# Optimization experiments

Hardware: AMD Instinct MI355X
Metric: run time of the kernel (lower is better)

Reference implementation:

```python
import jax, jax.numpy as jnp
import numpy as np
from jax import lax

CIN, COUT, K, PAD = 256, 128, 3, 1


def setup_inputs() -> dict:
    key = jax.random.key(0)
    ks = jax.random.split(key, 5)
    N, h0, w0 = 2, 64, 64
    x = jax.random.normal(ks[0], (N, CIN, h0, w0), jnp.float32)
    lateral_feat = jax.random.normal(ks[1], (N, COUT, 1, 1), jnp.float32)
    trans_w = jax.random.normal(ks[2], (CIN, COUT, K, K), jnp.float32) * 0.02
    off_w1 = jax.random.normal(ks[3], (64, COUT, 3, 3), jnp.float32) * 0.02
    off_b1 = jnp.zeros((64,), jnp.float32)
    off_w2 = jax.random.normal(ks[4], (2 * K * K, 64, 3, 3), jnp.float32) * 0.02
    off_b2 = jnp.zeros((2 * K * K,), jnp.float32)
    return dict(x=x, lateral_feat=lateral_feat, trans_w=trans_w,
                off_w1=off_w1, off_b1=off_b1, off_w2=off_w2, off_b2=off_b2)


def _conv2d(x, w, b, pad):
    y = lax.conv_general_dilated(x, w, (1, 1), [(pad, pad), (pad, pad)],
                                 dimension_numbers=('NCHW', 'OIHW', 'NCHW'))
    return y + b[None, :, None, None]


def _conv_transpose2d(x, w, stride, pad, out_pad):
    # torch ConvTranspose2d weight layout: [Cin, Cout, k, k]
    k = w.shape[2]
    wt = jnp.flip(w, (2, 3)).transpose(1, 0, 2, 3)  # [Cout, Cin, k, k]
    lo = k - 1 - pad
    hi = k - 1 - pad + out_pad
    return lax.conv_general_dilated(x, wt, (1, 1), [(lo, hi), (lo, hi)],
                                    lhs_dilation=(stride, stride),
                                    dimension_numbers=('NCHW', 'OIHW', 'NCHW'))


def _deform_conv2d(x, offset, w, pad):
    # x [N,C,H,W], offset [N,2*K*K,H,W] (y,x interleaved per kernel tap), w [O,C,K,K]
    N, C, H, W = x.shape
    O = w.shape[0]
    KK = K * K
    off = offset.reshape(N, KK, 2, H, W)
    ky = jnp.arange(KK) // K
    kx = jnp.arange(KK) % K
    py = jnp.arange(H)[None, None, :, None] + (ky - pad)[None, :, None, None] + off[:, :, 0]
    px = jnp.arange(W)[None, None, None, :] + (kx - pad)[None, :, None, None] + off[:, :, 1]
    y0 = jnp.floor(py)
    x0 = jnp.floor(px)
    dy = py - y0
    dx = px - x0
    y0i = y0.astype(jnp.int32)
    x0i = x0.astype(jnp.int32)
    xf = x.reshape(N, C, H * W)

    def corner(yi, xi, wgt):
        valid = (yi >= 0) & (yi < H) & (xi >= 0) & (xi < W)
        idx = (jnp.clip(yi, 0, H - 1) * W + jnp.clip(xi, 0, W - 1)).reshape(N, -1)
        v = jnp.take_along_axis(xf, idx[:, None, :], axis=2).reshape(N, C, KK, H, W)
        return v * (wgt * valid)[:, None]

    sampled = (corner(y0i, x0i, (1 - dy) * (1 - dx))
               + corner(y0i, x0i + 1, (1 - dy) * dx)
               + corner(y0i + 1, x0i, dy * (1 - dx))
               + corner(y0i + 1, x0i + 1, dy * dx))  # [N,C,KK,H,W]
    return jnp.einsum('nckhw,ock->nohw', sampled, w.reshape(O, C, KK))


def reference(x, lateral_feat, trans_w, off_w1, off_b1, off_w2, off_b2):
    up = _conv_transpose2d(x, trans_w, 2, PAD, 1)          # [N, COUT, 2h0, 2w0]
    h = jax.nn.relu(_conv2d(lateral_feat, off_w1, off_b1, 1))
    offset = jnp.tanh(_conv2d(h, off_w2, off_b2, 1))       # [N, 18, 1, 1]
    N, C, H, W = up.shape
    # offset.repeat(1, 1, H, W) with 1x1 spatial input == broadcast to full grid
    offset = jnp.broadcast_to(offset, (N, 2 * K * K, H, W))
    # deform_conv2d uses trans_conv weight [O=CIN, I=COUT, K, K], stride=1, pad=PAD
    return _deform_conv2d(up, offset, trans_w, PAD)        # [N, CIN, H, W]
```

## Files before the change

### kernel.cpp

```cpp
#include <hip/hip_runtime.h>
#include <hip/hip_bf16.h>
#include <math.h>

typedef __attribute__((ext_vector_type(8))) short s16x8;
typedef __attribute__((ext_vector_type(4))) float f32x4;

__device__ __forceinline__ unsigned short f2bf(float f) {
    union { float f; unsigned int u; } v; v.f = f;
    unsigned int u = v.u + 0x7FFFu + ((v.u >> 16) & 1u);
    return (unsigned short)(u >> 16);
}
__device__ __forceinline__ unsigned pk2(float lo, float hi) {
    __hip_bfloat162 h = __float22bfloat162_rn(make_float2(lo, hi));
    union { __hip_bfloat162 h; unsigned u; } v; v.h = h;
    return v.u;
}
__device__ __forceinline__ float blo(unsigned u) {
    union { unsigned u; float f; } v; v.u = u << 16; return v.f;
}
__device__ __forceinline__ float bhi(unsigned u) {
    union { unsigned u; float f; } v; v.u = u & 0xffff0000u; return v.f;
}

__device__ __forceinline__ void blend_store(uint4 uA, uint4 uB, uint4 uC, uint4 uD,
                                            float4 cw, unsigned short* dst) {
    unsigned ua[4] = {uA.x, uA.y, uA.z, uA.w};
    unsigned ub[4] = {uB.x, uB.y, uB.z, uB.w};
    unsigned uc[4] = {uC.x, uC.y, uC.z, uC.w};
    unsigned ud[4] = {uD.x, uD.y, uD.z, uD.w};
    unsigned pk[4];
#pragma unroll
    for (int i = 0; i < 4; ++i) {
        float vL = cw.x * blo(ua[i]) + cw.y * blo(ub[i]) + cw.z * blo(uc[i]) + cw.w * blo(ud[i]);
        float vH = cw.x * bhi(ua[i]) + cw.y * bhi(ub[i]) + cw.z * bhi(uc[i]) + cw.w * bhi(ud[i]);
        pk[i] = pk2(vL, vH);
    }
    *(uint4*)dst = make_uint4(pk[0], pk[1], pk[2], pk[3]);
}

__global__ __launch_bounds__(256) void k_prep(const float* __restrict__ x,
                                              const float* __restrict__ lat,
                                              const float* __restrict__ tw,
                                              const float* __restrict__ w1,
                                              const float* __restrict__ b1,
                                              const float* __restrict__ w2,
                                              const float* __restrict__ b2,
                                              unsigned short* __restrict__ xp,
                                              unsigned short* __restrict__ A2f,
                                              unsigned short* __restrict__ Awf,
                                              int* __restrict__ ipar,
                                              float* __restrict__ fpar) {
    __shared__ float sm[8420];
    int b = blockIdx.x, t = threadIdx.x;
    if (b == 0) {
        for (int i = t; i < 8192; i += 256) sm[(i >> 7) * 129 + (i & 127)] = w1[i * 9 + 4];
        __syncthreads();
        if (t < 128) {
            int n = t >> 6, o = t & 63;
            float s = b1[o];
            const float* ln = lat + n * 128;
#pragma unroll 8
            for (int c = 0; c < 128; ++c) s += ln[c] * sm[o * 129 + c];
            sm[8256 + t] = fmaxf(s, 0.f);
        }
        __syncthreads();
        if (t < 36) {
            int n = t / 18, j = t % 18;
            float s = b2[j];
            for (int o = 0; o < 64; ++o) s += sm[8256 + n * 64 + o] * w2[(j * 64 + o) * 9 + 4];
            float ov = tanhf(s);
            ov = fminf(fmaxf(ov, -0.999999f), 0.999999f);
            sm[8384 + t] = ov;
        }
        __syncthreads();
        if (t < 36) {
            int n = t / 18, j = t % 18;
            int tap = j >> 1, d = j & 1;
            float ov = sm[8384 + t];
            float fl = floorf(ov);
            int kc = d ? (tap % 3) : (tap / 3);
            ipar[(n * 9 + tap) * 2 + d] = kc - 1 + (int)fl;
            fpar[(n * 9 + tap) * 2 + d] = ov - fl;
        }
    } else if (b < 145) {
        int slot = (b - 1) * 256 + t;
        int l = slot & 63;
        int mi = (slot >> 6) & 3;
        int w = (slot >> 8) & 3;
        int k = slot >> 10;
        int row = w * 64 + mi * 16 + (l & 15);
        int kq = l >> 4;
        unsigned short v[8];
#pragma unroll
        for (int j = 0; j < 8; ++j) {
            int kcol = k * 32 + kq * 8 + j;
            int tap = kcol >> 7, c = kcol & 127;
            v[j] = f2bf(tw[(row * 128 + c) * 9 + tap]);
        }
        unsigned p0 = (unsigned)v[0] | ((unsigned)v[1] << 16);
        unsigned p1 = (unsigned)v[2] | ((unsigned)v[3] << 16);
        unsigned p2 = (unsigned)v[4] | ((unsigned)v[5] << 16);
        unsigned p3 = (unsigned)v[6] | ((unsigned)v[7] << 16);
        *(uint4*)(A2f + slot * 8) = make_uint4(p0, p1, p2, p3);
    } else if (b < 289) {
        int slot = (b - 145) * 256 + t;
        int l = slot & 63;
        int mi = (slot >> 6) & 3;
        int wm = (slot >> 8) & 1;
        int k = slot >> 9;
        int row = wm * 64 + mi * 16 + (l & 15);
        int kq = l >> 4;
        unsigned short v[8];
#pragma unroll
        for (int j = 0; j < 8; ++j) {
            int kcol = k * 32 + kq * 8 + j;
            int t9 = kcol >> 8, ci = kcol & 255;
            int ky = t9 / 3, kx = t9 - ky * 3;
            v[j] = f2bf(tw[(ci * 128 + row) * 9 + (2 - ky) * 3 + (2 - kx)]);
        }
        unsigned p0 = (unsigned)v[0] | ((unsigned)v[1] << 16);
        unsigned p1 = (unsigned)v[2] | ((unsigned)v[3] << 16);
        unsigned p2 = (unsigned)v[4] | ((unsigned)v[5] << 16);
        unsigned p3 = (unsigned)v[6] | ((unsigned)v[7] << 16);
        *(uint4*)(Awf + slot * 8) = make_uint4(p0, p1, p2, p3);
    } else {
        int bb = b - 289;
        int h = bb & 63, cq = (bb >> 6) & 3, n = bb >> 8;
        int c0 = cq * 64;
        {
            int wcol = t & 63, sub = t >> 6;
            for (int r = 0; r < 16; ++r) {
                int ci_l = r * 4 + sub;
                sm[ci_l * 65 + wcol] = x[((n * 256 + c0 + ci_l) * 64 + h) * 64 + wcol];
            }
        }
        __syncthreads();
        int wcol = t >> 2, cg = t & 3;
        unsigned short* dst = xp + (size_t)n * (65 * 65 * 256) + (h * 65 + wcol) * 256 + c0 + cg * 16;
        unsigned pk[8];
#pragma unroll
        for (int j = 0; j < 8; ++j)
            pk[j] = pk2(sm[(cg * 16 + 2 * j) * 65 + wcol], sm[(cg * 16 + 2 * j + 1) * 65 + wcol]);
        *(uint4*)dst = make_uint4(pk[0], pk[1], pk[2], pk[3]);
        *(uint4*)(dst + 8) = make_uint4(pk[4], pk[5], pk[6], pk[7]);
    }
}

__global__ __launch_bounds__(256) void k_tconv3(const unsigned short* __restrict__ xp,
                                                const unsigned short* __restrict__ Awf,
                                                unsigned short* __restrict__ upp) {
    __shared__ unsigned short Bs[2][64][40];
    __shared__ int st9[4];
    __shared__ int sbb[4];
    int t = threadIdx.x;
    int b = blockIdx.x;
    int phase = b >> 8, jj = b & 255;
    int n = jj >> 7, xpar = ((jj >> 6) & 1) ^ phase, yh = jj & 63;
    int y = yh * 2 + phase;
    const unsigned short* xpn = xp + (size_t)n * (65 * 65 * 256);

    int lane = t & 63, w = t >> 6;
    int col = lane & 15, q = lane >> 4;
    int wm = w >> 1, wn = w & 1;
    int bx = t >> 2, bcg = t & 3;
    int boff = bx * 256 + bcg * 8;

    int kys[2], kxs[2], nky, nkx;
    if (phase) { kys[0] = 0; kys[1] = 2; nky = 2; } else { kys[0] = 1; kys[1] = 1; nky = 1; }
    if (xpar)  { kxs[0] = 0; kxs[1] = 2; nkx = 2; } else { kxs[0] = 1; kxs[1] = 1; nkx = 1; }
    int nslots = nky * nkx;
    if (t < nslots) {
        int a1 = t / nkx, a2 = t % nkx;
        int ky = kys[a1], kx = kxs[a2];
        st9[t] = ky * 3 + kx;
        int d2 = (y + ky - 1) >> 1;
        int s = (xpar + kx - 1) >> 1;
        sbb[t] = (d2 * 65 + s) * 256;
    }
    int NT = nslots * 8;

    f32x4 acc[4][2];
#pragma unroll
    for (int mi = 0; mi < 4; ++mi)
#pragma unroll
        for (int ni = 0; ni < 2; ++ni) acc[mi][ni] = (f32x4){0.f, 0.f, 0.f, 0.f};

    __syncthreads();

    const unsigned short* Afw = Awf + wm * 2048 + lane * 8;
    s16x8 a_cur[4], a_nxt[4];

    {
        int kAw0 = st9[0] * 8;
        uint4 bv = *(const uint4*)(xpn + sbb[0] + boff);
        *(uint4*)&Bs[0][bx][bcg * 8] = bv;
#pragma unroll
        for (int mi = 0; mi < 4; ++mi)
            a_cur[mi] = *(const s16x8*)(Afw + kAw0 * 4096 + mi * 512);
    }
    __syncthreads();

    for (int cc = 0; cc < NT; ++cc) {
        int cc1 = cc + 1;
        uint4 bv;
        if (cc1 < NT) {
            int slot1 = cc1 >> 3, cb1 = cc1 & 7;
            int t9v = st9[slot1];
            int base = sbb[slot1];
            bv = *(const uint4*)(xpn + base + cb1 * 32 + boff);
            int kAw1 = t9v * 8 + cb1;
#pragma unroll
            for (int mi = 0; mi < 4; ++mi)
                a_nxt[mi] = *(const s16x8*)(Afw + kAw1 * 4096 + mi * 512);
        }
        s16x8 bb[2];
#pragma unroll
        for (int ni = 0; ni < 2; ++ni)
            bb[ni] = *(const s16x8*)&Bs[cc & 1][wn * 32 + ni * 16 + col][q * 8];
#pragma unroll
        for (int mi = 0; mi < 4; ++mi)
#pragma unroll
            for (int ni = 0; ni < 2; ++ni)
                acc[mi][ni] = __builtin_amdgcn_mfma_f32_16x16x32_bf16(a_cur[mi], bb[ni], acc[mi][ni], 0, 0, 0);
        if (cc1 < NT) {
            *(uint4*)&Bs[cc1 & 1][bx][bcg * 8] = bv;
#pragma unroll
            for (int mi = 0; mi < 4; ++mi) a_cur[mi] = a_nxt[mi];
        }
        __syncthreads();
    }

    unsigned short* uppn = upp + (size_t)n * (132 * 132 * 128);
#pragma unroll
    for (int mi = 0; mi < 4; ++mi)
#pragma unroll
        for (int ni = 0; ni < 2; ++ni) {
            int co = wm * 64 + mi * 16 + q * 4;
            int p64 = wn * 32 + ni * 16 + col;
            int xg = 2 * p64 + xpar;
            unsigned short* p = uppn + ((y + 2) * 132 + (xg + 2)) * 128 + co;
            unsigned lo = pk2(acc[mi][ni][0], acc[mi][ni][1]);
            unsigned hi = pk2(acc[mi][ni][2], acc[mi][ni][3]);
            *(uint2*)p = make_uint2(lo, hi);
        }
}

__global__ __launch_bounds__(256) void k_deform3(const unsigned short* __restrict__ upp,
                                                 const unsigned short* __restrict__ A2f,
                                                 const int* __restrict__ ipar,
                                                 const float* __restrict__ fpar,
                                                 float* __restrict__ out) {
    __shared__ unsigned short Bs[2][64][40];
    __shared__ int sbase[9];
    __shared__ float4 swt[9];
    int t = threadIdx.x;
    int b = blockIdx.x;
    int xcd = b & 7, j = b >> 3;
    int n = xcd >> 2, band = xcd & 3;
    int y = band * 32 + (j & 31);
    int tx0 = (j >> 5) * 64;
    const unsigned short* uppn = upp + (size_t)n * (132 * 132 * 128);

    int lane = t & 63, w = t >> 6;
    int col = lane & 15, q = lane >> 4;
    int bx = t >> 2, bcg = t & 3;
    int boff = bx * 128 + bcg * 8;

    if (t < 9) {
        int iy = ipar[(n * 9 + t) * 2 + 0], ix = ipar[(n * 9 + t) * 2 + 1];
        float fy = fpar[(n * 9 + t) * 2 + 0], fx = fpar[(n * 9 + t) * 2 + 1];
        sbase[t] = ((y + 2 + iy) * 132 + (tx0 + 2 + ix)) * 128;
        swt[t] = make_float4((1.f - fy) * (1.f - fx), (1.f - fy) * fx, fy * (1.f - fx), fy * fx);
    }

    f32x4 acc[4][4];
#pragma unroll
    for (int mi = 0; mi < 4; ++mi)
#pragma unroll
        for (int ni = 0; ni < 4; ++ni) acc[mi][ni] = (f32x4){0.f, 0.f, 0.f, 0.f};

    __syncthreads();

    const unsigned short* Afw = A2f + w * 2048 + lane * 8;
    s16x8 a_cur[4], a_nxt[4];

    {
        const unsigned short* p = uppn + sbase[0] + boff;
        uint4 uA = *(const uint4*)p;
        uint4 uB = *(const uint4*)(p + 128);
        uint4 uC = *(const uint4*)(p + 16896);
        uint4 uD = *(const uint4*)(p + 17024);
        blend_store(uA, uB, uC, uD, swt[0], &Bs[0][bx][bcg * 8]);
#pragma unroll
        for (int mi = 0; mi < 4; ++mi)
            a_cur[mi] = *(const s16x8*)(Afw + mi * 512);
    }
    __syncthreads();

#pragma unroll 2
    for (int k = 0; k < 36; ++k) {
        int k1 = k + 1;
        uint4 uA, uB, uC, uD;
        float4 cw;
        if (k1 < 36) {
            int t1 = k1 >> 2, cb1 = (k1 & 3) * 32;
            int base = sbase[t1];
            cw = swt[t1];
            const unsigned short* p = uppn + base + cb1 + boff;
            uA = *(const uint4*)p;
            uB = *(const uint4*)(p + 128);
            uC = *(const uint4*)(p + 16896);
            uD = *(const uint4*)(p + 17024);
#pragma unroll
            for (int mi = 0; mi < 4; ++mi)
                a_nxt[mi] = *(const s16x8*)(Afw + k1 * 8192 + mi * 512);
        }
        s16x8 bb[4];
#pragma unroll
        for (int ni = 0; ni < 4; ++ni)
            bb[ni] = *(const s16x8*)&Bs[k & 1][ni * 16 + col][q * 8];
#pragma unroll
        for (int mi = 0; mi < 4; ++mi)
#pragma unroll
            for (int ni = 0; ni < 4; ++ni)
                acc[mi][ni] = __builtin_amdgcn_mfma_f32_16x16x32_bf16(a_cur[mi], bb[ni], acc[mi][ni], 0, 0, 0);
        if (k1 < 36) {
            blend_store(uA, uB, uC, uD, cw, &Bs[k1 & 1][bx][bcg * 8]);
#pragma unroll
            for (int mi = 0; mi < 4; ++mi) a_cur[mi] = a_nxt[mi];
        }
        __syncthreads();
    }

#pragma unroll
    for (int mi = 0; mi < 4; ++mi)
#pragma unroll
        for (int ni = 0; ni < 4; ++ni) {
            int o = w * 64 + mi * 16 + q * 4;
            int xg = tx0 + ni * 16 + col;
            float* p = out + (((size_t)(n * 256 + o)) * 128 + y) * 128 + xg;
            p[0]         = acc[mi][ni][0];
            p[16384]     = acc[mi][ni][1];
            p[2 * 16384] = acc[mi][ni][2];
            p[3 * 16384] = acc[mi][ni][3];
        }
}

extern "C" void kernel_launch(void* const* d_in, const int* in_sizes, int n_in,
                              void* d_out, int out_size, void* d_ws, size_t ws_size,
                              hipStream_t stream) {
    const float* x   = (const float*)d_in[0];
    const float* lat = (const float*)d_in[1];
    const float* tw  = (const float*)d_in[2];
    const float* w1  = (const float*)d_in[3];
    const float* b1  = (const float*)d_in[4];
    const float* w2  = (const float*)d_in[5];
    const float* b2  = (const float*)d_in[6];
    float* out = (float*)d_out;

    char* ws = (char*)d_ws;
    unsigned short* upp = (unsigned short*)ws;
    unsigned short* xp  = (unsigned short*)(ws + 8921088);
    unsigned short* A2f = (unsigned short*)(ws + 13247488);
    unsigned short* Awf = (unsigned short*)(ws + 13837312);
    int*   ipar         = (int*)(ws + 14427136);
    float* fpar         = (float*)(ws + 14427424);

    hipMemsetAsync(ws, 0, 13247488, stream);
    k_prep<<<801, 256, 0, stream>>>(x, lat, tw, w1, b1, w2, b2, xp, A2f, Awf, ipar, fpar);
    k_tconv3<<<512, 256, 0, stream>>>(xp, Awf, upp);
    k_deform3<<<512, 256, 0, stream>>>(upp, A2f, ipar, fpar, out);
}
```

Before: 150.4 us.

## Restructure tconv to register-direct MFMA and deepen deform pipeline

```diff
diff --git a/kernel.cpp b/kernel.cpp
--- a/kernel.cpp
+++ b/kernel.cpp
@@ -4,6 +4,7 @@
 
 typedef __attribute__((ext_vector_type(8))) short s16x8;
 typedef __attribute__((ext_vector_type(4))) float f32x4;
+typedef __attribute__((ext_vector_type(2))) float v2f;
 
 __device__ __forceinline__ unsigned short f2bf(float f) {
     union { float f; unsigned int u; } v; v.f = f;
@@ -15,15 +16,15 @@
     union { __hip_bfloat162 h; unsigned u; } v; v.h = h;
     return v.u;
 }
-__device__ __forceinline__ float blo(unsigned u) {
-    union { unsigned u; float f; } v; v.u = u << 16; return v.f;
-}
-__device__ __forceinline__ float bhi(unsigned u) {
-    union { unsigned u; float f; } v; v.u = u & 0xffff0000u; return v.f;
-}
-
-__device__ __forceinline__ void blend_store(uint4 uA, uint4 uB, uint4 uC, uint4 uD,
-                                            float4 cw, unsigned short* dst) {
+__device__ __forceinline__ v2f up2(unsigned u) {
+    union { unsigned u; float f; } a, b;
+    a.u = u << 16; b.u = u & 0xffff0000u;
+    v2f r; r.x = a.f; r.y = b.f; return r;
+}
+
+__device__ __forceinline__ void blend4(uint4 uA, uint4 uB, uint4 uC, uint4 uD,
+                                       v2f c00, v2f c01, v2f c10, v2f c11,
+                                       unsigned short* dst) {
     unsigned ua[4] = {uA.x, uA.y, uA.z, uA.w};
     unsigned ub[4] = {uB.x, uB.y, uB.z, uB.w};
     unsigned uc[4] = {uC.x, uC.y, uC.z, uC.w};
@@ -31,9 +32,8 @@
     unsigned pk[4];
 #pragma unroll
     for (int i = 0; i < 4; ++i) {
-        float vL = cw.x * blo(ua[i]) + cw.y * blo(ub[i]) + cw.z * blo(uc[i]) + cw.w * blo(ud[i]);
-        float vH = cw.x * bhi(ua[i]) + cw.y * bhi(ub[i]) + cw.z * bhi(uc[i]) + cw.w * bhi(ud[i]);
-        pk[i] = pk2(vL, vH);
+        v2f r = c00 * up2(ua[i]) + c01 * up2(ub[i]) + c10 * up2(uc[i]) + c11 * up2(ud[i]);
+        pk[i] = pk2(r.x, r.y);
     }
     *(uint4*)dst = make_uint4(pk[0], pk[1], pk[2], pk[3]);
 }
@@ -146,113 +146,73 @@
     }
 }
 
-__global__ __launch_bounds__(256) void k_tconv3(const unsigned short* __restrict__ xp,
+__global__ __launch_bounds__(256) void k_tconv4(const unsigned short* __restrict__ xp,
                                                 const unsigned short* __restrict__ Awf,
                                                 unsigned short* __restrict__ upp) {
-    __shared__ unsigned short Bs[2][64][40];
-    __shared__ int st9[4];
-    __shared__ int sbb[4];
     int t = threadIdx.x;
     int b = blockIdx.x;
-    int phase = b >> 8, jj = b & 255;
-    int n = jj >> 7, xpar = ((jj >> 6) & 1) ^ phase, yh = jj & 63;
-    int y = yh * 2 + phase;
+    int cls = b >> 7;
+    int phase = (cls < 2) ? 1 : 0;
+    int xpar = 1 - (cls & 1);
+    int idx = b & 127;
+    int n = idx >> 6, yh = idx & 63;
+    int y = 2 * yh + phase;
     const unsigned short* xpn = xp + (size_t)n * (65 * 65 * 256);
 
     int lane = t & 63, w = t >> 6;
     int col = lane & 15, q = lane >> 4;
-    int wm = w >> 1, wn = w & 1;
-    int bx = t >> 2, bcg = t & 3;
-    int boff = bx * 256 + bcg * 8;
-
-    int kys[2], kxs[2], nky, nkx;
-    if (phase) { kys[0] = 0; kys[1] = 2; nky = 2; } else { kys[0] = 1; kys[1] = 1; nky = 1; }
-    if (xpar)  { kxs[0] = 0; kxs[1] = 2; nkx = 2; } else { kxs[0] = 1; kxs[1] = 1; nkx = 1; }
-    int nslots = nky * nkx;
-    if (t < nslots) {
-        int a1 = t / nkx, a2 = t % nkx;
-        int ky = kys[a1], kx = kxs[a2];
-        st9[t] = ky * 3 + kx;
+    int pos = w * 16 + col;
+
+    int nky = phase ? 2 : 1;
+    int nkx = xpar ? 2 : 1;
+
+    f32x4 acc[8];
+#pragma unroll
+    for (int mi = 0; mi < 8; ++mi) acc[mi] = (f32x4){0.f, 0.f, 0.f, 0.f};
+
+    const unsigned short* Afl = Awf + lane * 8;
+
+    for (int a1 = 0; a1 < nky; ++a1) {
+        int ky = phase ? (a1 ? 2 : 0) : 1;
         int d2 = (y + ky - 1) >> 1;
-        int s = (xpar + kx - 1) >> 1;
-        sbb[t] = (d2 * 65 + s) * 256;
-    }
-    int NT = nslots * 8;
-
-    f32x4 acc[4][2];
-#pragma unroll
-    for (int mi = 0; mi < 4; ++mi)
-#pragma unroll
-        for (int ni = 0; ni < 2; ++ni) acc[mi][ni] = (f32x4){0.f, 0.f, 0.f, 0.f};
-
-    __syncthreads();
-
-    const unsigned short* Afw = Awf + wm * 2048 + lane * 8;
-    s16x8 a_cur[4], a_nxt[4];
-
-    {
-        int kAw0 = st9[0] * 8;
-        uint4 bv = *(const uint4*)(xpn + sbb[0] + boff);
-        *(uint4*)&Bs[0][bx][bcg * 8] = bv;
-#pragma unroll
-        for (int mi = 0; mi < 4; ++mi)
-            a_cur[mi] = *(const s16x8*)(Afw + kAw0 * 4096 + mi * 512);
-    }
-    __syncthreads();
-
-    for (int cc = 0; cc < NT; ++cc) {
-        int cc1 = cc + 1;
-        uint4 bv;
-        if (cc1 < NT) {
-            int slot1 = cc1 >> 3, cb1 = cc1 & 7;
-            int t9v = st9[slot1];
-            int base = sbb[slot1];
-            bv = *(const uint4*)(xpn + base + cb1 * 32 + boff);
-            int kAw1 = t9v * 8 + cb1;
-#pragma unroll
-            for (int mi = 0; mi < 4; ++mi)
-                a_nxt[mi] = *(const s16x8*)(Afw + kAw1 * 4096 + mi * 512);
-        }
-        s16x8 bb[2];
-#pragma unroll
-        for (int ni = 0; ni < 2; ++ni)
-            bb[ni] = *(const s16x8*)&Bs[cc & 1][wn * 32 + ni * 16 + col][q * 8];
-#pragma unroll
-        for (int mi = 0; mi < 4; ++mi)
-#pragma unroll
-            for (int ni = 0; ni < 2; ++ni)
-                acc[mi][ni] = __builtin_amdgcn_mfma_f32_16x16x32_bf16(a_cur[mi], bb[ni], acc[mi][ni], 0, 0, 0);
-        if (cc1 < NT) {
-            *(uint4*)&Bs[cc1 & 1][bx][bcg * 8] = bv;
-#pragma unroll
-            for (int mi = 0; mi < 4; ++mi) a_cur[mi] = a_nxt[mi];
-        }
-        __syncthreads();
+        for (int a2 = 0; a2 < nkx; ++a2) {
+            int kx = xpar ? (a2 ? 2 : 0) : 1;
+            int s = (xpar + kx - 1) >> 1;
+            int t9 = ky * 3 + kx;
+            const unsigned short* bptr = xpn + ((size_t)(d2 * 65 + s + pos)) * 256 + q * 8;
+            const unsigned short* aptr = Afl + t9 * 8 * 4096;
+#pragma unroll 2
+            for (int cb = 0; cb < 8; ++cb) {
+                s16x8 bf = *(const s16x8*)(bptr + cb * 32);
+                s16x8 a[8];
+#pragma unroll
+                for (int mi = 0; mi < 8; ++mi)
+                    a[mi] = *(const s16x8*)(aptr + cb * 4096 + (mi >> 2) * 2048 + (mi & 3) * 512);
+#pragma unroll
+                for (int mi = 0; mi < 8; ++mi)
+                    acc[mi] = __builtin_amdgcn_mfma_f32_16x16x32_bf16(a[mi], bf, acc[mi], 0, 0, 0);
+            }
+        }
     }
 
     unsigned short* uppn = upp + (size_t)n * (132 * 132 * 128);
-#pragma unroll
-    for (int mi = 0; mi < 4; ++mi)
-#pragma unroll
-        for (int ni = 0; ni < 2; ++ni) {
-            int co = wm * 64 + mi * 16 + q * 4;
-            int p64 = wn * 32 + ni * 16 + col;
-            int xg = 2 * p64 + xpar;
-            unsigned short* p = uppn + ((y + 2) * 132 + (xg + 2)) * 128 + co;
-            unsigned lo = pk2(acc[mi][ni][0], acc[mi][ni][1]);
-            unsigned hi = pk2(acc[mi][ni][2], acc[mi][ni][3]);
-            *(uint2*)p = make_uint2(lo, hi);
-        }
-}
-
-__global__ __launch_bounds__(256) void k_deform3(const unsigned short* __restrict__ upp,
-                                                 const unsigned short* __restrict__ A2f,
-                                                 const int* __restrict__ ipar,
-                                                 const float* __restrict__ fpar,
-                                                 float* __restrict__ out) {
-    __shared__ unsigned short Bs[2][64][40];
-    __shared__ int sbase[9];
-    __shared__ float4 swt[9];
+    int xg = 2 * pos + xpar;
+#pragma unroll
+    for (int mi = 0; mi < 8; ++mi) {
+        int co = mi * 16 + q * 4;
+        unsigned short* p = uppn + ((y + 2) * 132 + (xg + 2)) * 128 + co;
+        unsigned lo = pk2(acc[mi][0], acc[mi][1]);
+        unsigned hi = pk2(acc[mi][2], acc[mi][3]);
+        *(uint2*)p = make_uint2(lo, hi);
+    }
+}
+
+__global__ __launch_bounds__(256, 2) void k_deform4(const unsigned short* __restrict__ upp,
+                                                    const unsigned short* __restrict__ A2f,
+                                                    const int* __restrict__ ipar,
+                                                    const float* __restrict__ fpar,
+                                                    float* __restrict__ out) {
+    __shared__ unsigned short Bs[2][64][84];
     int t = threadIdx.x;
     int b = blockIdx.x;
     int xcd = b & 7, j = b >> 3;
@@ -266,12 +226,8 @@
     int bx = t >> 2, bcg = t & 3;
     int boff = bx * 128 + bcg * 8;
 
-    if (t < 9) {
-        int iy = ipar[(n * 9 + t) * 2 + 0], ix = ipar[(n * 9 + t) * 2 + 1];
-        float fy = fpar[(n * 9 + t) * 2 + 0], fx = fpar[(n * 9 + t) * 2 + 1];
-        sbase[t] = ((y + 2 + iy) * 132 + (tx0 + 2 + ix)) * 128;
-        swt[t] = make_float4((1.f - fy) * (1.f - fx), (1.f - fy) * fx, fy * (1.f - fx), fy * fx);
-    }
+    const int* ipn = ipar + n * 18;
+    const float* fpn = fpar + n * 18;
 
     f32x4 acc[4][4];
 #pragma unroll
@@ -279,58 +235,98 @@
 #pragma unroll
         for (int ni = 0; ni < 4; ++ni) acc[mi][ni] = (f32x4){0.f, 0.f, 0.f, 0.f};
 
+    const unsigned short* Afw = A2f + w * 2048 + lane * 8;
+
+#define TAPP(tap, PB, C00, C01, C10, C11)                                        \
+    {                                                                            \
+        int iy = ipn[(tap)*2], ix = ipn[(tap)*2 + 1];                            \
+        float fy = fpn[(tap)*2], fx = fpn[(tap)*2 + 1];                          \
+        float w00 = (1.f - fy) * (1.f - fx), w01 = (1.f - fy) * fx;              \
+        float w10 = fy * (1.f - fx), w11 = fy * fx;                              \
+        C00 = (v2f){w00, w00}; C01 = (v2f){w01, w01};                            \
+        C10 = (v2f){w10, w10}; C11 = (v2f){w11, w11};                            \
+        PB = uppn + ((size_t)((y + 2 + iy) * 132 + (tx0 + 2 + ix))) * 128 + boff;\
+    }
+
+    const unsigned short* pb;
+    v2f cN00, cN01, cN10, cN11;
+    uint4 cr[8];
+    s16x8 a_cur[8], a_nxt[8];
+
+    TAPP(0, pb, cN00, cN01, cN10, cN11);
+#pragma unroll
+    for (int c = 0; c < 2; ++c) {
+        const unsigned short* p = pb + c * 32;
+        cr[c * 4 + 0] = *(const uint4*)p;
+        cr[c * 4 + 1] = *(const uint4*)(p + 128);
+        cr[c * 4 + 2] = *(const uint4*)(p + 16896);
+        cr[c * 4 + 3] = *(const uint4*)(p + 17024);
+    }
+#pragma unroll
+    for (int c = 0; c < 2; ++c)
+#pragma unroll
+        for (int mi = 0; mi < 4; ++mi)
+            a_cur[c * 4 + mi] = *(const s16x8*)(Afw + c * 8192 + mi * 512);
+#pragma unroll
+    for (int c = 0; c < 2; ++c)
+        blend4(cr[c * 4 + 0], cr[c * 4 + 1], cr[c * 4 + 2], cr[c * 4 + 3],
+               cN00, cN01, cN10, cN11, &Bs[0][bx][c * 42 + bcg * 8]);
+#pragma unroll
+    for (int c = 0; c < 2; ++c) {
+        const unsigned short* p = pb + 64 + c * 32;
+        cr[c * 4 + 0] = *(const uint4*)p;
+        cr[c * 4 + 1] = *(const uint4*)(p + 128);
+        cr[c * 4 + 2] = *(const uint4*)(p + 16896);
+        cr[c * 4 + 3] = *(const uint4*)(p + 17024);
+    }
     __syncthreads();
 
-    const unsigned short* Afw = A2f + w * 2048 + lane * 8;
-    s16x8 a_cur[4], a_nxt[4];
-
-    {
-        const unsigned short* p = uppn + sbase[0] + boff;
-        uint4 uA = *(const uint4*)p;
-        uint4 uB = *(const uint4*)(p + 128);
-        uint4 uC = *(const uint4*)(p + 16896);
-        uint4 uD = *(const uint4*)(p + 17024);
-        blend_store(uA, uB, uC, uD, swt[0], &Bs[0][bx][bcg * 8]);
-#pragma unroll
-        for (int mi = 0; mi < 4; ++mi)
-            a_cur[mi] = *(const s16x8*)(Afw + mi * 512);
-    }
-    __syncthreads();
-
 #pragma unroll 2
-    for (int k = 0; k < 36; ++k) {
-        int k1 = k + 1;
-        uint4 uA, uB, uC, uD;
-        float4 cw;
-        if (k1 < 36) {
-            int t1 = k1 >> 2, cb1 = (k1 & 3) * 32;
-            int base = sbase[t1];
-            cw = swt[t1];
-            const unsigned short* p = uppn + base + cb1 + boff;
-            uA = *(const uint4*)p;
-            uB = *(const uint4*)(p + 128);
-            uC = *(const uint4*)(p + 16896);
-            uD = *(const uint4*)(p + 17024);
+    for (int kk = 0; kk < 18; ++kk) {
+        int cur = kk & 1;
+        if (kk < 17) {
+#pragma unroll
+            for (int c = 0; c < 2; ++c)
+                blend4(cr[c * 4 + 0], cr[c * 4 + 1], cr[c * 4 + 2], cr[c * 4 + 3],
+                       cN00, cN01, cN10, cN11, &Bs[cur ^ 1][bx][c * 42 + bcg * 8]);
+#pragma unroll
+            for (int c = 0; c < 2; ++c)
+#pragma unroll
+                for (int mi = 0; mi < 4; ++mi)
+                    a_nxt[c * 4 + mi] = *(const s16x8*)(Afw + (size_t)(2 * (kk + 1) + c) * 8192 + mi * 512);
+        }
+        if (kk < 16) {
+            int kk2 = kk + 2;
+            TAPP(kk2 >> 1, pb, cN00, cN01, cN10, cN11);
+            int cb0 = (kk2 & 1) ? 64 : 0;
+#pragma unroll
+            for (int c = 0; c < 2; ++c) {
+                const unsigned short* p = pb + cb0 + c * 32;
+                cr[c * 4 + 0] = *(const uint4*)p;
+                cr[c * 4 + 1] = *(const uint4*)(p + 128);
+                cr[c * 4 + 2] = *(const uint4*)(p + 16896);
+                cr[c * 4 + 3] = *(const uint4*)(p + 17024);
+            }
+        }
+#pragma unroll
+        for (int c = 0; c < 2; ++c) {
+            s16x8 bbf[4];
+#pragma unroll
+            for (int ni = 0; ni < 4; ++ni)
+                bbf[ni] = *(const s16x8*)&Bs[cur][ni * 16 + col][c * 42 + q * 8];
 #pragma unroll
             for (int mi = 0; mi < 4; ++mi)
-                a_nxt[mi] = *(const s16x8*)(Afw + k1 * 8192 + mi * 512);
-        }
-        s16x8 bb[4];
-#pragma unroll
-        for (int ni = 0; ni < 4; ++ni)
-            bb[ni] = *(const s16x8*)&Bs[k & 1][ni * 16 + col][q * 8];
-#pragma unroll
-        for (int mi = 0; mi < 4; ++mi)
-#pragma unroll
-            for (int ni = 0; ni < 4; ++ni)
-                acc[mi][ni] = __builtin_amdgcn_mfma_f32_16x16x32_bf16(a_cur[mi], bb[ni], acc[mi][ni], 0, 0, 0);
-        if (k1 < 36) {
-            blend_store(uA, uB, uC, uD, cw, &Bs[k1 & 1][bx][bcg * 8]);
-#pragma unroll
-            for (int mi = 0; mi < 4; ++mi) a_cur[mi] = a_nxt[mi];
-        }
-        __syncthreads();
-    }
+#pragma unroll
+                for (int ni = 0; ni < 4; ++ni)
+                    acc[mi][ni] = __builtin_amdgcn_mfma_f32_16x16x32_bf16(a_cur[c * 4 + mi], bbf[ni], acc[mi][ni], 0, 0, 0);
+        }
+        if (kk < 17) {
+#pragma unroll
+            for (int i = 0; i < 8; ++i) a_cur[i] = a_nxt[i];
+        }
+        __syncthreads();
+    }
+#undef TAPP
 
 #pragma unroll
     for (int mi = 0; mi < 4; ++mi)
@@ -368,6 +364,6 @@
 
     hipMemsetAsync(ws, 0, 13247488, stream);
     k_prep<<<801, 256, 0, stream>>>(x, lat, tw, w1, b1, w2, b2, xp, A2f, Awf, ipar, fpar);
-    k_tconv3<<<512, 256, 0, stream>>>(xp, Awf, upp);
-    k_deform3<<<512, 256, 0, stream>>>(upp, A2f, ipar, fpar, out);
-}
+    k_tconv4<<<512, 256, 0, stream>>>(xp, Awf, upp);
+    k_deform4<<<512, 256, 0, stream>>>(upp, A2f, ipar, fpar, out);
+}
```

Measured after the change: 157.9 us. 5.0% more time.
